# Performance work log

Measured on AMD Instinct MI355X. Metric: run time of the kernel, lower is better.

The kernel has to match this reference:

```python
import jax, jax.numpy as jnp
import numpy as np

CODEBOOK_DIM = 12          # log2(codebook_size)
CODEBOOK_SIZE = 4096
DIM = 512
INV_TEMPERATURE = 100.0
CODEBOOK_SCALE = 1.0
DIVERSITY_GAMMA = 1.0
ENTROPY_LOSS_WEIGHT = 0.1
EPS = 1e-5


def setup_inputs() -> dict:
    key = jax.random.key(0)
    k_x, k_wi, k_wo = jax.random.split(key, 3)
    x = jax.random.normal(k_x, (4, 4096, DIM), dtype=jnp.float32)
    # nn.Linear weights: (out_features, in_features)
    w_in = jax.random.normal(k_wi, (CODEBOOK_DIM, DIM), dtype=jnp.float32) * 0.02
    b_in = jnp.zeros((CODEBOOK_DIM,), dtype=jnp.float32)
    w_out = jax.random.normal(k_wo, (DIM, CODEBOOK_DIM), dtype=jnp.float32) * 0.02
    b_out = jnp.zeros((DIM,), dtype=jnp.float32)
    return {"x": x, "w_in": w_in, "b_in": b_in, "w_out": w_out, "b_out": b_out}


def _entropy(prob):
    return (-prob * jnp.log(jnp.clip(prob, EPS))).sum(axis=-1)


def _make_codebook():
    mask = (2 ** jnp.arange(CODEBOOK_DIM - 1, -1, -1)).astype(jnp.int32)  # [d]
    all_codes = jnp.arange(CODEBOOK_SIZE, dtype=jnp.int32)
    bits = ((all_codes[:, None] & mask) != 0).astype(jnp.float32)  # [cs, d]
    codebook = bits * CODEBOOK_SCALE * 2 - CODEBOOK_SCALE  # {-1, +1}
    return mask, codebook


def reference(x, w_in, b_in, w_out, b_out):
    mask, codebook = _make_codebook()

    # project in: [b, n, dim] -> [b, n, d]
    xp = jnp.einsum('bnd,cd->bnc', x, w_in) + b_in  # c == codebook_dim here

    # sign quantization (num_codebooks = 1, so c-dim is implicit)
    quantized = jnp.where(xp > 0, CODEBOOK_SCALE, -CODEBOOK_SCALE).astype(xp.dtype)
    indices = ((quantized > 0).astype(jnp.int32) * mask).sum(axis=-1)  # [b, n]

    # straight-through estimator (training path)
    x_st = xp + jax.lax.stop_gradient(quantized - xp)

    # entropy aux loss over full codebook (frac_per_sample_entropy = 1.0)
    flat = xp.reshape(-1, CODEBOOK_DIM)  # original (pre-quant) input, [bn, d]
    # -distance * inv_temp = 2 * inv_temp * <x, code>
    logits = (2.0 * INV_TEMPERATURE) * (flat @ codebook.T)  # [bn, cs]
    prob = jax.nn.softmax(logits, axis=-1)
    per_sample_entropy = _entropy(prob).mean()
    avg_prob = prob.mean(axis=0)  # [cs]
    codebook_entropy = _entropy(avg_prob)
    entropy_aux_loss = per_sample_entropy - DIVERSITY_GAMMA * codebook_entropy
    aux_loss = entropy_aux_loss * ENTROPY_LOSS_WEIGHT

    # project out: [b, n, d] -> [b, n, dim]
    out = jnp.einsum('bnc,dc->bnd', x_st, w_out) + b_out
    return out, indices, aux_loss
```

## Files before the change

### kernel.cpp

```cpp
#include <hip/hip_runtime.h>
#include <hip/hip_bf16.h>


#define NS    16384
#define NOUT  (NS*512)
#define AUXO  (NOUT+NS)
#define INVT2 200.0f
#define NBLK  256

__global__ __launch_bounds__(512, 2) void k_main(
    const float* __restrict__ x,
    const float* __restrict__ w_in,  const float* __restrict__ b_in,
    const float* __restrict__ w_out, const float* __restrict__ b_out,
    float* __restrict__ out, float* __restrict__ idx_out,
    float* __restrict__ P, float* __restrict__ Csum) {

  __shared__ float s_wi[6144];
  __shared__ float s_wt[6144];
  __shared__ float s_phi[64][64];
  __shared__ float s_psi[64][64];
  __shared__ float s_xp[8][8][12];
  __shared__ float s_h[8];

  const int t = threadIdx.x;

  for (int k = 0; k < 12; ++k) {
    int f  = t + k * 512;
    int kk = f & 3;
    int q  = f >> 2;
    int sub = q & 15, e4 = (q >> 4) & 7, d = q >> 7;
    int e  = sub * 32 + e4 * 4 + kk;
    s_wi[f] = w_in[d * 512 + e];
    s_wt[f] = w_out[e * 12 + d];
  }
  __syncthreads();

  const int wave = t >> 6, lane = t & 63;
  const int g = lane >> 4, sub = lane & 15;

  float bin[12];
  #pragma unroll
  for (int d = 0; d < 12; ++d) bin[d] = b_in[d];

  const int i0 = blockIdx.x * 64 + wave * 8 + g;
  const int i1 = i0 + 4;

  const float4* xr0 = (const float4*)(x + (size_t)i0 * 512 + sub * 32);
  const float4* xr1 = (const float4*)(x + (size_t)i1 * 512 + sub * 32);
  float4 xv0[8], xv1[8];
  #pragma unroll
  for (int e4 = 0; e4 < 8; ++e4) { xv0[e4] = xr0[e4]; xv1[e4] = xr1[e4]; }

  float p0[12], p1[12];
  #pragma unroll
  for (int d = 0; d < 12; ++d) { p0[d] = 0.f; p1[d] = 0.f; }
  #pragma unroll
  for (int e4 = 0; e4 < 8; ++e4) {
    #pragma unroll
    for (int d = 0; d < 12; ++d) {
      float4 w4 = ((const float4*)s_wi)[d * 128 + e4 * 16 + sub];
      p0[d] += xv0[e4].x * w4.x + xv0[e4].y * w4.y + xv0[e4].z * w4.z + xv0[e4].w * w4.w;
      p1[d] += xv1[e4].x * w4.x + xv1[e4].y * w4.y + xv1[e4].z * w4.z + xv1[e4].w * w4.w;
    }
  }
  #pragma unroll
  for (int d = 0; d < 12; ++d) {
    #pragma unroll
    for (int m = 1; m <= 8; m <<= 1) {
      p0[d] += __shfl_xor(p0[d], m, 16);
      p1[d] += __shfl_xor(p1[d], m, 16);
    }
    p0[d] += bin[d];
    p1[d] += bin[d];
  }

  unsigned idx0 = 0u, idx1 = 0u;
  #pragma unroll
  for (int d = 0; d < 12; ++d) {
    idx0 |= (p0[d] > 0.f ? 1u : 0u) << (11 - d);
    idx1 |= (p1[d] > 0.f ? 1u : 0u) << (11 - d);
  }
  if (sub == 0) {
    idx_out[i0] = (float)idx0;
    idx_out[i1] = (float)idx1;
    #pragma unroll
    for (int d = 0; d < 12; ++d) {
      s_xp[wave][g][d]     = p0[d];
      s_xp[wave][4 + g][d] = p1[d];
    }
  }

  float sg0[12], sg1[12];
  #pragma unroll
  for (int d = 0; d < 12; ++d) {
    sg0[d] = p0[d] > 0.f ? 1.f : -1.f;
    sg1[d] = p1[d] > 0.f ? 1.f : -1.f;
  }
  #pragma unroll
  for (int e4 = 0; e4 < 8; ++e4) {
    float4 bo = ((const float4*)b_out)[sub * 8 + e4];
    float4 o0 = bo, o1 = bo;
    #pragma unroll
    for (int d = 0; d < 12; ++d) {
      float4 w4 = ((const float4*)s_wt)[d * 128 + e4 * 16 + sub];
      o0.x += sg0[d] * w4.x; o0.y += sg0[d] * w4.y; o0.z += sg0[d] * w4.z; o0.w += sg0[d] * w4.w;
      o1.x += sg1[d] * w4.x; o1.y += sg1[d] * w4.y; o1.z += sg1[d] * w4.z; o1.w += sg1[d] * w4.w;
    }
    ((float4*)(out + (size_t)i0 * 512 + sub * 32))[e4] = o0;
    ((float4*)(out + (size_t)i1 * 512 + sub * 32))[e4] = o1;
  }

  float hacc = 0.f;
  #pragma unroll 1
  for (int s = 0; s < 8; ++s) {
    float xq[12];
    #pragma unroll
    for (int d = 0; d < 12; ++d) xq[d] = s_xp[wave][s][d];

    float hi = 0.f, lo = 0.f, ah = 0.f, al = 0.f;
    #pragma unroll
    for (int d = 0; d < 6; ++d) {
      int bh = (lane >> (5 - d)) & 1;
      hi += bh ? xq[d]     : -xq[d];
      lo += bh ? xq[6 + d] : -xq[6 + d];
      ah += fabsf(xq[d]);
      al += fabsf(xq[6 + d]);
    }
    float lhi = INVT2 * (hi - ah);
    float llo = INVT2 * (lo - al);
    float ehi = __expf(lhi);
    float elo = __expf(llo);
    float Shi = ehi, Slo = elo;
    #pragma unroll
    for (int m = 1; m <= 32; m <<= 1) {
      Shi += __shfl_xor(Shi, m);
      Slo += __shfl_xor(Slo, m);
    }
    float phi = ehi / Shi;
    float psi = elo / Slo;
    float lnShi = __logf(Shi), lnSlo = __logf(Slo);
    hacc += phi * (lhi - lnShi) + psi * (llo - lnSlo);

    const int ws = wave * 8 + s;
    s_phi[ws][lane] = phi;
    s_psi[ws][lane] = psi;
  }

  #pragma unroll
  for (int m = 1; m <= 32; m <<= 1) hacc += __shfl_xor(hacc, m);
  if (lane == 0) s_h[wave] = hacc;
  __syncthreads();
  if (t == 0) {
    float hs = 0.f;
    for (int w2 = 0; w2 < 8; ++w2) hs += s_h[w2];
    atomicAdd(Csum, hs);
  }

  const int jb = (t >> 5) * 4;
  const int lb = (t & 31) * 2;
  float a00 = 0.f, a01 = 0.f, a10 = 0.f, a11 = 0.f;
  float a20 = 0.f, a21 = 0.f, a30 = 0.f, a31 = 0.f;
  #pragma unroll 4
  for (int s = 0; s < 64; ++s) {
    float4 ph = *(const float4*)&s_phi[s][jb];
    float2 ps = *(const float2*)&s_psi[s][lb];
    a00 += ph.x * ps.x; a01 += ph.x * ps.y;
    a10 += ph.y * ps.x; a11 += ph.y * ps.y;
    a20 += ph.z * ps.x; a21 += ph.z * ps.y;
    a30 += ph.w * ps.x; a31 += ph.w * ps.y;
  }
  float* Pr = P + (size_t)blockIdx.x * 4096;
  *(float2*)&Pr[(jb + 0) * 64 + lb] = make_float2(a00, a01);
  *(float2*)&Pr[(jb + 1) * 64 + lb] = make_float2(a10, a11);
  *(float2*)&Pr[(jb + 2) * 64 + lb] = make_float2(a20, a21);
  *(float2*)&Pr[(jb + 3) * 64 + lb] = make_float2(a30, a31);
}

__global__ __launch_bounds__(256) void k_reduce(const float* __restrict__ P,
                                                float* __restrict__ Esum) {
  __shared__ float red[16][17];
  __shared__ float ered[16];
  const int t = threadIdx.x;
  const int cl = t & 15, rg = t >> 4;
  const int c = blockIdx.x * 16 + cl;
  float s = 0.f;
  #pragma unroll
  for (int k = 0; k < 16; ++k) s += P[(size_t)(rg + k * 16) * 4096 + c];
  red[rg][cl] = s;
  __syncthreads();
  if (t < 16) {
    float tot = 0.f;
    #pragma unroll
    for (int r = 0; r < 16; ++r) tot += red[r][t];
    float pb = tot * (1.f / (float)NS);
    ered[t] = pb * __logf(fmaxf(pb, 1e-5f));
  }
  __syncthreads();
  if (t == 0) {
    float e = 0.f;
    #pragma unroll
    for (int r = 0; r < 16; ++r) e += ered[r];
    atomicAdd(Esum, e);
  }
}

__global__ void k_final(const float* __restrict__ Csum, const float* __restrict__ Esum,
                        float* __restrict__ aux) {
  if (threadIdx.x == 0) {
    float per_sample_entropy = -Csum[0] * (1.f / (float)NS);
    float codebook_entropy   = -Esum[0];
    aux[0] = 0.1f * (per_sample_entropy - codebook_entropy);
  }
}

extern "C" void kernel_launch(void* const* d_in, const int* in_sizes, int n_in,
                              void* d_out, int out_size, void* d_ws, size_t ws_size,
                              hipStream_t stream) {
  const float* x     = (const float*)d_in[0];
  const float* w_in  = (const float*)d_in[1];
  const float* b_in  = (const float*)d_in[2];
  const float* w_out = (const float*)d_in[3];
  const float* b_out = (const float*)d_in[4];
  float* out = (float*)d_out;

  float* P    = (float*)d_ws;
  float* scal = (float*)((char*)d_ws + (size_t)NBLK * 4096 * 4);

  hipMemsetAsync(scal, 0, 2 * sizeof(float), stream);
  k_main<<<NBLK, 512, 0, stream>>>(x, w_in, b_in, w_out, b_out,
                                   out, out + NOUT, P, scal);
  k_reduce<<<256, 256, 0, stream>>>(P, scal + 1);
  k_final<<<1, 64, 0, stream>>>(scal, scal + 1, out + AUXO);
}
```

Baseline: 120.0 us.

## Coalesce x loads and output stores, process rows sequentially, tighten launch bounds

Both weight tables are now kept in LDS in natural row-major order. The x loads are made fully coalesced: each 16-lane group now reads contiguous 64-float chunks instead of a 32-float slice per lane. The output projection is restructured so each wave writes whole 512-float rows with contiguous float4 stores. Rows are processed one at a time to cut register pressure, launch bounds are raised to 4 blocks per SIMD-level budget, the s_xp buffer is folded into s_phi, and the per-block entropy sum becomes a per-wave atomic. Risks are spilling under the tighter register cap, more atomics on the scalar, and reduced ILP from handling one row per iteration.

Measured after the change: 379.5 us. 3.16x slower.

```diff
diff --git a/kernel.cpp b/kernel.cpp
--- a/kernel.cpp
+++ b/kernel.cpp
@@ -8,114 +8,102 @@
 #define INVT2 200.0f
 #define NBLK  256
 
-__global__ __launch_bounds__(512, 2) void k_main(
+__global__ __launch_bounds__(512, 4) void k_main(
     const float* __restrict__ x,
     const float* __restrict__ w_in,  const float* __restrict__ b_in,
     const float* __restrict__ w_out, const float* __restrict__ b_out,
     float* __restrict__ out, float* __restrict__ idx_out,
     float* __restrict__ P, float* __restrict__ Csum) {
 
-  __shared__ float s_wi[6144];
-  __shared__ float s_wt[6144];
-  __shared__ float s_phi[64][64];
-  __shared__ float s_psi[64][64];
-  __shared__ float s_xp[8][8][12];
-  __shared__ float s_h[8];
+  __shared__ __align__(16) float s_wi[6144];
+  __shared__ __align__(16) float s_wt[6144];
+  __shared__ __align__(16) float s_phi[64][64];
+  __shared__ __align__(16) float s_psi[64][64];
 
   const int t = threadIdx.x;
 
+  #pragma unroll
   for (int k = 0; k < 12; ++k) {
-    int f  = t + k * 512;
-    int kk = f & 3;
-    int q  = f >> 2;
-    int sub = q & 15, e4 = (q >> 4) & 7, d = q >> 7;
-    int e  = sub * 32 + e4 * 4 + kk;
-    s_wi[f] = w_in[d * 512 + e];
+    int f = t + k * 512;
+    int d = f >> 9, e = f & 511;
+    s_wi[f] = w_in[f];
     s_wt[f] = w_out[e * 12 + d];
   }
   __syncthreads();
 
   const int wave = t >> 6, lane = t & 63;
   const int g = lane >> 4, sub = lane & 15;
+  const int ibase = blockIdx.x * 64 + wave * 8;
 
   float bin[12];
   #pragma unroll
   for (int d = 0; d < 12; ++d) bin[d] = b_in[d];
 
-  const int i0 = blockIdx.x * 64 + wave * 8 + g;
-  const int i1 = i0 + 4;
-
-  const float4* xr0 = (const float4*)(x + (size_t)i0 * 512 + sub * 32);
-  const float4* xr1 = (const float4*)(x + (size_t)i1 * 512 + sub * 32);
-  float4 xv0[8], xv1[8];
-  #pragma unroll
-  for (int e4 = 0; e4 < 8; ++e4) { xv0[e4] = xr0[e4]; xv1[e4] = xr1[e4]; }
-
-  float p0[12], p1[12];
-  #pragma unroll
-  for (int d = 0; d < 12; ++d) { p0[d] = 0.f; p1[d] = 0.f; }
-  #pragma unroll
-  for (int e4 = 0; e4 < 8; ++e4) {
+  #pragma unroll 1
+  for (int bt = 0; bt < 2; ++bt) {
+    const int i = ibase + bt * 4 + g;
+    float4 xv[8];
+    #pragma unroll
+    for (int e4 = 0; e4 < 8; ++e4)
+      xv[e4] = *(const float4*)(x + (size_t)i * 512 + e4 * 64 + sub * 4);
+
+    float p[12];
+    #pragma unroll
+    for (int d = 0; d < 12; ++d) p[d] = 0.f;
+    #pragma unroll
+    for (int e4 = 0; e4 < 8; ++e4) {
+      #pragma unroll
+      for (int d = 0; d < 12; ++d) {
+        float4 w4 = *(const float4*)&s_wi[d * 512 + e4 * 64 + sub * 4];
+        p[d] += xv[e4].x * w4.x + xv[e4].y * w4.y + xv[e4].z * w4.z + xv[e4].w * w4.w;
+      }
+    }
     #pragma unroll
     for (int d = 0; d < 12; ++d) {
-      float4 w4 = ((const float4*)s_wi)[d * 128 + e4 * 16 + sub];
-      p0[d] += xv0[e4].x * w4.x + xv0[e4].y * w4.y + xv0[e4].z * w4.z + xv0[e4].w * w4.w;
-      p1[d] += xv1[e4].x * w4.x + xv1[e4].y * w4.y + xv1[e4].z * w4.z + xv1[e4].w * w4.w;
-    }
-  }
-  #pragma unroll
-  for (int d = 0; d < 12; ++d) {
-    #pragma unroll
-    for (int m = 1; m <= 8; m <<= 1) {
-      p0[d] += __shfl_xor(p0[d], m, 16);
-      p1[d] += __shfl_xor(p1[d], m, 16);
-    }
-    p0[d] += bin[d];
-    p1[d] += bin[d];
-  }
-
-  unsigned idx0 = 0u, idx1 = 0u;
-  #pragma unroll
-  for (int d = 0; d < 12; ++d) {
-    idx0 |= (p0[d] > 0.f ? 1u : 0u) << (11 - d);
-    idx1 |= (p1[d] > 0.f ? 1u : 0u) << (11 - d);
-  }
-  if (sub == 0) {
-    idx_out[i0] = (float)idx0;
-    idx_out[i1] = (float)idx1;
+      #pragma unroll
+      for (int m = 1; m <= 8; m <<= 1) p[d] += __shfl_xor(p[d], m, 16);
+      p[d] += bin[d];
+    }
+
+    unsigned idx = 0u;
+    #pragma unroll
+    for (int d = 0; d < 12; ++d) idx |= (p[d] > 0.f ? 1u : 0u) << (11 - d);
+    if (sub == 0) {
+      idx_out[i] = (float)idx;
+      #pragma unroll
+      for (int d = 0; d < 12; ++d) s_phi[wave * 8 + bt * 4 + g][d] = p[d];
+    }
+  }
+
+  float4 bo0 = *(const float4*)(b_out + 4 * lane);
+  float4 bo1 = *(const float4*)(b_out + 256 + 4 * lane);
+  #pragma unroll 1
+  for (int s = 0; s < 8; ++s) {
+    const int i = ibase + s;
+    const float* xr = s_phi[wave * 8 + s];
+    float sg[12];
+    #pragma unroll
+    for (int d = 0; d < 12; ++d) sg[d] = xr[d] > 0.f ? 1.f : -1.f;
+
+    float4 o0 = bo0, o1 = bo1;
     #pragma unroll
     for (int d = 0; d < 12; ++d) {
-      s_xp[wave][g][d]     = p0[d];
-      s_xp[wave][4 + g][d] = p1[d];
-    }
-  }
-
-  float sg0[12], sg1[12];
-  #pragma unroll
-  for (int d = 0; d < 12; ++d) {
-    sg0[d] = p0[d] > 0.f ? 1.f : -1.f;
-    sg1[d] = p1[d] > 0.f ? 1.f : -1.f;
-  }
-  #pragma unroll
-  for (int e4 = 0; e4 < 8; ++e4) {
-    float4 bo = ((const float4*)b_out)[sub * 8 + e4];
-    float4 o0 = bo, o1 = bo;
-    #pragma unroll
-    for (int d = 0; d < 12; ++d) {
-      float4 w4 = ((const float4*)s_wt)[d * 128 + e4 * 16 + sub];
-      o0.x += sg0[d] * w4.x; o0.y += sg0[d] * w4.y; o0.z += sg0[d] * w4.z; o0.w += sg0[d] * w4.w;
-      o1.x += sg1[d] * w4.x; o1.y += sg1[d] * w4.y; o1.z += sg1[d] * w4.z; o1.w += sg1[d] * w4.w;
-    }
-    ((float4*)(out + (size_t)i0 * 512 + sub * 32))[e4] = o0;
-    ((float4*)(out + (size_t)i1 * 512 + sub * 32))[e4] = o1;
+      float4 wa = *(const float4*)&s_wt[d * 512 + 4 * lane];
+      float4 wb = *(const float4*)&s_wt[d * 512 + 256 + 4 * lane];
+      o0.x += sg[d] * wa.x; o0.y += sg[d] * wa.y; o0.z += sg[d] * wa.z; o0.w += sg[d] * wa.w;
+      o1.x += sg[d] * wb.x; o1.y += sg[d] * wb.y; o1.z += sg[d] * wb.z; o1.w += sg[d] * wb.w;
+    }
+    *(float4*)(out + (size_t)i * 512 + 4 * lane)       = o0;
+    *(float4*)(out + (size_t)i * 512 + 256 + 4 * lane) = o1;
   }
 
   float hacc = 0.f;
   #pragma unroll 1
   for (int s = 0; s < 8; ++s) {
+    const int ws = wave * 8 + s;
     float xq[12];
     #pragma unroll
-    for (int d = 0; d < 12; ++d) xq[d] = s_xp[wave][s][d];
+    for (int d = 0; d < 12; ++d) xq[d] = s_phi[ws][d];
 
     float hi = 0.f, lo = 0.f, ah = 0.f, al = 0.f;
     #pragma unroll
@@ -141,20 +129,14 @@
     float lnShi = __logf(Shi), lnSlo = __logf(Slo);
     hacc += phi * (lhi - lnShi) + psi * (llo - lnSlo);
 
-    const int ws = wave * 8 + s;
     s_phi[ws][lane] = phi;
     s_psi[ws][lane] = psi;
   }
-
   #pragma unroll
   for (int m = 1; m <= 32; m <<= 1) hacc += __shfl_xor(hacc, m);
-  if (lane == 0) s_h[wave] = hacc;
-  __syncthreads();
-  if (t == 0) {
-    float hs = 0.f;
-    for (int w2 = 0; w2 < 8; ++w2) hs += s_h[w2];
-    atomicAdd(Csum, hs);
-  }
+  if (lane == 0) atomicAdd(Csum, hacc);
+
+  __syncthreads();
 
   const int jb = (t >> 5) * 4;
   const int lb = (t & 31) * 2;
```
